# Performance work log

Measured on AMD Instinct MI355X. Metric: run time of the kernel, lower is better.

## Reference

```python
import jax, jax.numpy as jnp
import numpy as np

CLIP_LENGTH = 256.0
NUM_CLASSES = 21
OVERLAP_THRESH = 0.5
GAMMA = 2.0
ALPHA = 0.25
EPS = float(np.finfo(np.float32).eps)

B, K, N_GT = 32, 32768, 32


def setup_inputs() -> dict:
    key = jax.random.key(0)
    ks = jax.random.split(key, 9)
    loc_data = jax.random.uniform(ks[0], (B, K, 2), jnp.float32) * 64.0 + 1.0  # frame-unit offsets
    conf_data = jax.random.normal(ks[1], (B, K, NUM_CLASSES), jnp.float32)
    prop_loc_data = jax.random.normal(ks[2], (B, K, 2), jnp.float32)
    prop_conf_data = jax.random.normal(ks[3], (B, K, NUM_CLASSES), jnp.float32)
    center_data = jax.random.normal(ks[4], (B, K, 1), jnp.float32)
    priors = jax.random.uniform(ks[5], (K, 1), jnp.float32)  # normalized centers in [0,1]
    t0 = jax.random.uniform(ks[6], (B, N_GT), jnp.float32) * 0.8
    dur = jax.random.uniform(ks[7], (B, N_GT), jnp.float32) * 0.18 + 0.02
    t1 = jnp.minimum(t0 + dur, 1.0)
    labels = jax.random.randint(ks[8], (B, N_GT), 1, NUM_CLASSES).astype(jnp.float32)
    targets = jnp.stack([t0, t1, labels], axis=-1)  # [B, N, 3]
    return {"loc_data": loc_data, "conf_data": conf_data, "prop_loc_data": prop_loc_data,
            "prop_conf_data": prop_conf_data, "center_data": center_data,
            "priors": priors, "targets": targets}


def _calc_iou(pred, target):
    pl, pr = pred[..., 0], pred[..., 1]
    tl, tr = target[..., 0], target[..., 1]
    inter = jnp.minimum(pl, tl) + jnp.minimum(pr, tr)
    union = (pl + pr) + (tl + tr) - inter
    return inter / jnp.maximum(union, EPS)


def _giou_loss(pred, target):
    pl, pr = pred[..., 0], pred[..., 1]
    tl, tr = target[..., 0], target[..., 1]
    inter = jnp.minimum(pl, tl) + jnp.minimum(pr, tr)
    union = (pl + pr) + (tl + tr) - inter
    ious = inter / jnp.maximum(union, EPS)
    ac = jnp.maximum(pl, tl) + jnp.maximum(pr, tr)
    gious = ious - (ac - union) / jnp.maximum(ac, EPS)
    return 1.0 - gious


_ALPHA_VEC = jnp.full((NUM_CLASSES,), 1.0 - ALPHA, jnp.float32).at[0].set(ALPHA)


def _focal_sum(logits, tgt):
    # FocalLoss_Ori with pre-softmax inside MultiSegmentLoss; reduction=sum
    probs = jax.nn.softmax(logits, axis=-1)
    pt = jnp.take_along_axis(probs, tgt[..., None], axis=-1)[..., 0] + 1e-10
    return (-_ALPHA_VEC[tgt] * (1.0 - pt) ** GAMMA * jnp.log(pt)).sum()


def _match_targets(loc_data_ng, priors, targets):
    # everything here mirrors the torch.no_grad() matching block
    truths = targets[..., :2]                       # [B,N,2]
    labels = targets[..., 2].astype(jnp.int32)      # [B,N]
    center = priors[:, 0]                           # [K]
    left = (center[None, :, None] - truths[:, None, :, 0]) * CLIP_LENGTH   # [B,K,N]
    right = (truths[:, None, :, 1] - center[None, :, None]) * CLIP_LENGTH  # [B,K,N]
    maxn = CLIP_LENGTH * 2.0
    area = jnp.where((left < 0) | (right < 0), maxn, left + right)
    best_area = area.min(-1)                        # [B,K]
    best_idx = area.argmin(-1)                      # [B,K]
    t0 = jnp.take_along_axis(truths[..., 0], best_idx, axis=1)
    t1 = jnp.take_along_axis(truths[..., 1], best_idx, axis=1)
    loc_t = jnp.stack([(center[None, :] - t0) * CLIP_LENGTH,
                       (t1 - center[None, :]) * CLIP_LENGTH], axis=-1)     # [B,K,2]
    conf_t = jnp.take_along_axis(labels, best_idx, axis=1)
    conf_t = jnp.where(best_area >= maxn, 0, conf_t)                       # [B,K]
    iou = _calc_iou(loc_data_ng, loc_t)
    prop_conf_t = jnp.where(iou < OVERLAP_THRESH, 0, conf_t)
    prop_w = loc_data_ng[..., 0] + loc_data_ng[..., 1]
    prop_loc_t = (loc_t - loc_data_ng) / (0.5 * prop_w[..., None])
    return loc_t, conf_t, prop_loc_t, prop_conf_t


def reference(loc_data, conf_data, prop_loc_data, prop_conf_data, center_data, priors, targets):
    loc_t, conf_t, prop_loc_t, prop_conf_t = _match_targets(
        jax.lax.stop_gradient(loc_data), priors, targets)

    pos = conf_t > 0
    posf = pos.astype(loc_data.dtype)
    N = jnp.maximum(posf.sum(), 1.0)
    prop_pos = prop_conf_t > 0
    ppf = prop_pos.astype(loc_data.dtype)
    PN = jnp.maximum(ppf.sum(), 1.0)

    # GIoU localization loss over positives
    loss_l = (_giou_loss(loc_data, loc_t) * posf).sum() / N

    # L1 proposal refinement loss over proposal positives
    loss_prop_l = (jnp.abs(prop_loc_data - prop_loc_t).sum(-1) * ppf).sum() / PN

    # centerness BCE-with-logits against refined IoU, over positives
    prop_pre_w = loc_data[..., 0:1] + loc_data[..., 1:2]
    cur_loc_p = 0.5 * prop_pre_w * prop_loc_data + loc_data
    ious_ct = jnp.maximum(_calc_iou(cur_loc_p, loc_t), 0.0)
    x = center_data[..., 0]
    bce = jnp.maximum(x, 0.0) - x * ious_ct + jnp.log1p(jnp.exp(-jnp.abs(x)))
    loss_ct = (bce * posf).sum() / N

    # focal classification losses over all anchors
    loss_c = _focal_sum(conf_data, conf_t) / N
    loss_prop_c = _focal_sum(prop_conf_data, prop_conf_t) / PN

    return (loss_l, loss_c, loss_prop_l, loss_prop_c, loss_ct)
```

## Files before the change

### kernel.cpp

```cpp
#include <hip/hip_runtime.h>
#include <math.h>

#define NCLS 21
#define NGT 32
#define CLIPLEN 256.0f
#define MAXN 512.0f
#define FEPS 1.1920928955078125e-07f


typedef float f32x4 __attribute__((ext_vector_type(4)));
typedef f32x4 f32x4_u __attribute__((aligned(4)));

__device__ __forceinline__ float fastrcp(float x) { return __builtin_amdgcn_rcpf(x); }

__device__ __forceinline__ void load_row21(const float* __restrict__ p, float* r) {
    f32x4 v0 = *(const f32x4_u*)(p + 0);
    f32x4 v1 = *(const f32x4_u*)(p + 4);
    f32x4 v2 = *(const f32x4_u*)(p + 8);
    f32x4 v3 = *(const f32x4_u*)(p + 12);
    f32x4 v4 = *(const f32x4_u*)(p + 16);
    float  v5 = p[20];
    r[0]=v0.x; r[1]=v0.y; r[2]=v0.z; r[3]=v0.w;
    r[4]=v1.x; r[5]=v1.y; r[6]=v1.z; r[7]=v1.w;
    r[8]=v2.x; r[9]=v2.y; r[10]=v2.z; r[11]=v2.w;
    r[12]=v3.x; r[13]=v3.y; r[14]=v3.z; r[15]=v3.w;
    r[16]=v4.x; r[17]=v4.y; r[18]=v4.z; r[19]=v4.w;
    r[20]=v5;
}

__device__ __forceinline__ float focal_reg(const float* r, int tgt) {
    float m0 = fmaxf(fmaxf(r[0],  r[1]),  r[2]);
    float m1 = fmaxf(fmaxf(r[3],  r[4]),  r[5]);
    float m2 = fmaxf(fmaxf(r[6],  r[7]),  r[8]);
    float m3 = fmaxf(fmaxf(r[9],  r[10]), r[11]);
    float m4 = fmaxf(fmaxf(r[12], r[13]), r[14]);
    float m5 = fmaxf(fmaxf(r[15], r[16]), r[17]);
    float m6 = fmaxf(fmaxf(r[18], r[19]), r[20]);
    float ma = fmaxf(fmaxf(m0, m1), m2);
    float mb = fmaxf(fmaxf(m3, m4), m5);
    float m  = fmaxf(fmaxf(ma, mb), m6);

    float e[NCLS];
#pragma unroll
    for (int i = 0; i < NCLS; ++i) e[i] = __expf(r[i] - m);
    float s0 = (e[0] + e[1])  + (e[2] + e[3]);
    float s1 = (e[4] + e[5])  + (e[6] + e[7]);
    float s2 = (e[8] + e[9])  + (e[10] + e[11]);
    float s3 = (e[12] + e[13]) + (e[14] + e[15]);
    float s4 = (e[16] + e[17]) + (e[18] + e[19]);
    float s  = ((s0 + s1) + (s2 + s3)) + (s4 + e[20]);

    float rt = 0.0f;
#pragma unroll
    for (int i = 0; i < NCLS; ++i) rt = (i == tgt) ? r[i] : rt;

    float pt  = __expf(rt - m) * fastrcp(s) + 1e-10f;
    float lpt = __logf(pt);
    float a   = (tgt == 0) ? 0.25f : 0.75f;
    float om  = 1.0f - pt;
    return -a * om * om * lpt;
}

template <bool PARTIALS>
__global__ __launch_bounds__(256, 5) void msl_main(
    const float* __restrict__ loc_data,
    const float* __restrict__ conf_data,
    const float* __restrict__ prop_loc_data,
    const float* __restrict__ prop_conf_data,
    const float* __restrict__ center_data,
    const float* __restrict__ priors,
    const float* __restrict__ targets,
    double* __restrict__ ws,
    int K, int nblk)
{
    __shared__ float s_red[6 * 4];

    const int b    = blockIdx.y;
    const int tid  = threadIdx.x;
    const int lane = tid & 63;
    const int w    = tid >> 6;
    const int k    = blockIdx.x * 256 + tid;
    const size_t idx = (size_t)b * K + k;

    const float  c   = priors[k];
    const float2 loc = ((const float2*)loc_data)[idx];
    const float2 plo = ((const float2*)prop_loc_data)[idx];
    const float  x   = center_data[idx];

    float rc[NCLS], rp[NCLS];
    load_row21(conf_data      + idx * NCLS, rc);
    load_row21(prop_conf_data + idx * NCLS, rp);

    const float* tgs = targets + (size_t)b * (NGT * 3);
    float bestA = 3.0e38f;
    float bT0 = 0.0f, bT1 = 0.0f, bLb = 0.0f;
#pragma unroll
    for (int n = 0; n < NGT; ++n) {
        const float t0n = tgs[3 * n];
        const float t1n = tgs[3 * n + 1];
        const float lbn = tgs[3 * n + 2];
        const bool outside = (t0n > c) || (t1n < c);
        const float cand = outside ? MAXN : (t1n - t0n) * CLIPLEN;
        const bool better = cand < bestA;
        bestA = better ? cand : bestA;
        bT0   = better ? t0n  : bT0;
        bT1   = better ? t1n  : bT1;
        bLb   = better ? lbn  : bLb;
    }
    const float tl = (c - bT0) * CLIPLEN;
    const float tr = (bT1 - c) * CLIPLEN;
    const int conf_t = (bestA >= MAXN) ? 0 : (int)bLb;

    const float pl = loc.x, pr = loc.y;

    const float inter = fminf(pl, tl) + fminf(pr, tr);
    const float uni   = pl + pr + tl + tr - inter;
    const float iou   = inter * fastrcp(fmaxf(uni, FEPS));

    const int prop_conf_t = (iou < 0.5f) ? 0 : conf_t;
    const float posf = (conf_t > 0) ? 1.0f : 0.0f;
    const float ppf  = (prop_conf_t > 0) ? 1.0f : 0.0f;

    const float ac   = fmaxf(pl, tl) + fmaxf(pr, tr);
    const float giou = iou - (ac - uni) * fastrcp(fmaxf(ac, FEPS));
    const float v_ll = (1.0f - giou) * posf;

    const float prop_w = pl + pr;
    const float inv_hw = 2.0f * fastrcp(prop_w);
    const float plt0 = (tl - pl) * inv_hw;
    const float plt1 = (tr - pr) * inv_hw;
    const float v_lpl = (fabsf(plo.x - plt0) + fabsf(plo.y - plt1)) * ppf;

    const float cur0 = 0.5f * prop_w * plo.x + pl;
    const float cur1 = 0.5f * prop_w * plo.y + pr;
    const float in2  = fminf(cur0, tl) + fminf(cur1, tr);
    const float un2  = cur0 + cur1 + tl + tr - in2;
    const float iou2 = fmaxf(in2 * fastrcp(fmaxf(un2, FEPS)), 0.0f);
    const float ebx  = __expf(-fabsf(x));
    const float bce  = fmaxf(x, 0.0f) - x * iou2 + __logf(1.0f + ebx);
    const float v_ct = bce * posf;

    const float v_lc  = focal_reg(rc, conf_t);
    const float v_lpc = focal_reg(rp, prop_conf_t);

    float vals[6] = { v_ll, v_lc, v_lpl, v_lpc, v_ct, posf + 4096.0f * ppf };
#pragma unroll
    for (int i = 0; i < 6; ++i) {
        float v = vals[i];
#pragma unroll
        for (int off = 32; off > 0; off >>= 1) v += __shfl_xor(v, off);
        if (lane == 0) s_red[i * 4 + w] = v;
    }
    __syncthreads();
    if (tid == 0) {
        const int blk = blockIdx.y * gridDim.x + blockIdx.x;
#pragma unroll
        for (int i = 0; i < 5; ++i) {
            double s = (double)s_red[i * 4 + 0] + (double)s_red[i * 4 + 1]
                     + (double)s_red[i * 4 + 2] + (double)s_red[i * 4 + 3];
            if (PARTIALS) ws[(size_t)i * nblk + blk] = s;
            else          atomicAdd(&ws[i], s);
        }
        double ct = (double)s_red[5 * 4 + 0] + (double)s_red[5 * 4 + 1]
                  + (double)s_red[5 * 4 + 2] + (double)s_red[5 * 4 + 3];
        double pp = floor(ct / 4096.0);
        double ps = ct - 4096.0 * pp;
        if (PARTIALS) {
            ws[(size_t)5 * nblk + blk] = ps;
            ws[(size_t)6 * nblk + blk] = pp;
        } else {
            atomicAdd(&ws[5], ps);
            atomicAdd(&ws[6], pp);
        }
    }
}

__global__ __launch_bounds__(256) void msl_reduce(
    const double* __restrict__ p, int nblk, float* __restrict__ out)
{
    __shared__ double s_acc[7];
    __shared__ double s_w[4];
    const int tid  = threadIdx.x;
    const int lane = tid & 63;
    const int w    = tid >> 6;

    for (int i = 0; i < 7; ++i) {
        double v = 0.0;
        for (int j = tid; j < nblk; j += 256) v += p[(size_t)i * nblk + j];
#pragma unroll
        for (int off = 32; off > 0; off >>= 1) v += __shfl_xor(v, off);
        if (lane == 0) s_w[w] = v;
        __syncthreads();
        if (tid == 0) s_acc[i] = s_w[0] + s_w[1] + s_w[2] + s_w[3];
        __syncthreads();
    }
    if (tid == 0) {
        const double N  = fmax(s_acc[5], 1.0);
        const double PN = fmax(s_acc[6], 1.0);
        out[0] = (float)(s_acc[0] / N);
        out[1] = (float)(s_acc[1] / N);
        out[2] = (float)(s_acc[2] / PN);
        out[3] = (float)(s_acc[3] / PN);
        out[4] = (float)(s_acc[4] / N);
    }
}

__global__ void msl_finalize(const double* __restrict__ acc, float* __restrict__ out) {
    const double N  = fmax(acc[5], 1.0);
    const double PN = fmax(acc[6], 1.0);
    out[0] = (float)(acc[0] / N);
    out[1] = (float)(acc[1] / N);
    out[2] = (float)(acc[2] / PN);
    out[3] = (float)(acc[3] / PN);
    out[4] = (float)(acc[4] / N);
}

extern "C" void kernel_launch(void* const* d_in, const int* in_sizes, int n_in,
                              void* d_out, int out_size, void* d_ws, size_t ws_size,
                              hipStream_t stream) {
    const float* loc_data       = (const float*)d_in[0];
    const float* conf_data      = (const float*)d_in[1];
    const float* prop_loc_data  = (const float*)d_in[2];
    const float* prop_conf_data = (const float*)d_in[3];
    const float* center_data    = (const float*)d_in[4];
    const float* priors         = (const float*)d_in[5];
    const float* targets        = (const float*)d_in[6];
    float* out = (float*)d_out;

    const int K = in_sizes[5];
    const int B = in_sizes[6] / (NGT * 3);
    const int nblk = (K / 256) * B;

    double* ws = (double*)d_ws;
    dim3 grid(K / 256, B);

    if (ws_size >= (size_t)7 * nblk * sizeof(double)) {
        msl_main<true><<<grid, 256, 0, stream>>>(loc_data, conf_data, prop_loc_data,
                                                 prop_conf_data, center_data, priors,
                                                 targets, ws, K, nblk);
        msl_reduce<<<1, 256, 0, stream>>>(ws, nblk, out);
    } else {
        hipMemsetAsync(ws, 0, 7 * sizeof(double), stream);
        msl_main<false><<<grid, 256, 0, stream>>>(loc_data, conf_data, prop_loc_data,
                                                  prop_conf_data, center_data, priors,
                                                  targets, ws, K, nblk);
        msl_finalize<<<1, 1, 0, stream>>>(ws, out);
    }
}
```

Measured before the change: 69.03 us.

## Process four batch slices per thread with double-buffered register prefetch

The main kernel is replaced by one where each thread handles the same anchor across four batch slices. It loads the next slice's rows into a second register buffer while computing the current one, so memory latency is software-pipelined. This cuts the block count and the number of partial sums by four, and the prior value is reused across slices. In exchange, register pressure roughly doubles (launch bounds drop to 3 waves per SIMD), which may lower occupancy. A separate fallback kernel with the atomic path is kept for shapes that do not divide evenly.

```diff
diff --git a/kernel.cpp b/kernel.cpp
--- a/kernel.cpp
+++ b/kernel.cpp
@@ -3,6 +3,7 @@
 
 #define NCLS 21
 #define NGT 32
+#define NITER 4
 #define CLIPLEN 256.0f
 #define MAXN 512.0f
 #define FEPS 1.1920928955078125e-07f
@@ -61,37 +62,10 @@
     return -a * om * om * lpt;
 }
 
-template <bool PARTIALS>
-__global__ __launch_bounds__(256, 5) void msl_main(
-    const float* __restrict__ loc_data,
-    const float* __restrict__ conf_data,
-    const float* __restrict__ prop_loc_data,
-    const float* __restrict__ prop_conf_data,
-    const float* __restrict__ center_data,
-    const float* __restrict__ priors,
-    const float* __restrict__ targets,
-    double* __restrict__ ws,
-    int K, int nblk)
+__device__ __forceinline__ void anchor_accum(
+    const float* __restrict__ tgs, float c, float2 loc, float2 plo, float x,
+    const float* rc, const float* rp, float* a6)
 {
-    __shared__ float s_red[6 * 4];
-
-    const int b    = blockIdx.y;
-    const int tid  = threadIdx.x;
-    const int lane = tid & 63;
-    const int w    = tid >> 6;
-    const int k    = blockIdx.x * 256 + tid;
-    const size_t idx = (size_t)b * K + k;
-
-    const float  c   = priors[k];
-    const float2 loc = ((const float2*)loc_data)[idx];
-    const float2 plo = ((const float2*)prop_loc_data)[idx];
-    const float  x   = center_data[idx];
-
-    float rc[NCLS], rp[NCLS];
-    load_row21(conf_data      + idx * NCLS, rc);
-    load_row21(prop_conf_data + idx * NCLS, rp);
-
-    const float* tgs = targets + (size_t)b * (NGT * 3);
     float bestA = 3.0e38f;
     float bT0 = 0.0f, bT1 = 0.0f, bLb = 0.0f;
 #pragma unroll
@@ -140,38 +114,156 @@
     const float bce  = fmaxf(x, 0.0f) - x * iou2 + __logf(1.0f + ebx);
     const float v_ct = bce * posf;
 
-    const float v_lc  = focal_reg(rc, conf_t);
-    const float v_lpc = focal_reg(rp, prop_conf_t);
-
-    float vals[6] = { v_ll, v_lc, v_lpl, v_lpc, v_ct, posf + 4096.0f * ppf };
+    a6[0] += v_ll;
+    a6[1] += focal_reg(rc, conf_t);
+    a6[2] += v_lpl;
+    a6[3] += focal_reg(rp, prop_conf_t);
+    a6[4] += v_ct;
+    a6[5] += posf + 4096.0f * ppf;
+}
+
+__global__ __launch_bounds__(256, 3) void msl_pipe(
+    const float* __restrict__ loc_data,
+    const float* __restrict__ conf_data,
+    const float* __restrict__ prop_loc_data,
+    const float* __restrict__ prop_conf_data,
+    const float* __restrict__ center_data,
+    const float* __restrict__ priors,
+    const float* __restrict__ targets,
+    double* __restrict__ ws,
+    int K, int GB, int nblk)
+{
+    __shared__ float s_red[6 * 4];
+
+    const int tid  = threadIdx.x;
+    const int lane = tid & 63;
+    const int w    = tid >> 6;
+    const int T    = blockIdx.x * 256 + tid;
+    const int b0   = T / K;
+    const int k    = T - b0 * K;
+    const size_t step = (size_t)GB * K;
+
+    const float c = priors[k];
+
+    float rcA[NCLS], rpA[NCLS], rcB[NCLS], rpB[NCLS];
+    float2 locA, ploA, locB, ploB;
+    float xA, xB;
+    float a6[6] = {0, 0, 0, 0, 0, 0};
+
+    const size_t i0 = (size_t)T;
+    locA = ((const float2*)loc_data)[i0];
+    ploA = ((const float2*)prop_loc_data)[i0];
+    xA   = center_data[i0];
+    load_row21(conf_data      + i0 * NCLS, rcA);
+    load_row21(prop_conf_data + i0 * NCLS, rpA);
+
+    {
+        const size_t i1 = i0 + step;
+        locB = ((const float2*)loc_data)[i1];
+        ploB = ((const float2*)prop_loc_data)[i1];
+        xB   = center_data[i1];
+        load_row21(conf_data      + i1 * NCLS, rcB);
+        load_row21(prop_conf_data + i1 * NCLS, rpB);
+        anchor_accum(targets + (size_t)b0 * (NGT * 3), c, locA, ploA, xA, rcA, rpA, a6);
+    }
+    {
+        const size_t i2 = i0 + 2 * step;
+        locA = ((const float2*)loc_data)[i2];
+        ploA = ((const float2*)prop_loc_data)[i2];
+        xA   = center_data[i2];
+        load_row21(conf_data      + i2 * NCLS, rcA);
+        load_row21(prop_conf_data + i2 * NCLS, rpA);
+        anchor_accum(targets + (size_t)(b0 + GB) * (NGT * 3), c, locB, ploB, xB, rcB, rpB, a6);
+    }
+    {
+        const size_t i3 = i0 + 3 * step;
+        locB = ((const float2*)loc_data)[i3];
+        ploB = ((const float2*)prop_loc_data)[i3];
+        xB   = center_data[i3];
+        load_row21(conf_data      + i3 * NCLS, rcB);
+        load_row21(prop_conf_data + i3 * NCLS, rpB);
+        anchor_accum(targets + (size_t)(b0 + 2 * GB) * (NGT * 3), c, locA, ploA, xA, rcA, rpA, a6);
+    }
+    anchor_accum(targets + (size_t)(b0 + 3 * GB) * (NGT * 3), c, locB, ploB, xB, rcB, rpB, a6);
+
 #pragma unroll
     for (int i = 0; i < 6; ++i) {
-        float v = vals[i];
+        float v = a6[i];
 #pragma unroll
         for (int off = 32; off > 0; off >>= 1) v += __shfl_xor(v, off);
         if (lane == 0) s_red[i * 4 + w] = v;
     }
     __syncthreads();
     if (tid == 0) {
-        const int blk = blockIdx.y * gridDim.x + blockIdx.x;
+        const int blk = blockIdx.x;
 #pragma unroll
         for (int i = 0; i < 5; ++i) {
             double s = (double)s_red[i * 4 + 0] + (double)s_red[i * 4 + 1]
                      + (double)s_red[i * 4 + 2] + (double)s_red[i * 4 + 3];
-            if (PARTIALS) ws[(size_t)i * nblk + blk] = s;
-            else          atomicAdd(&ws[i], s);
+            ws[(size_t)i * nblk + blk] = s;
         }
         double ct = (double)s_red[5 * 4 + 0] + (double)s_red[5 * 4 + 1]
                   + (double)s_red[5 * 4 + 2] + (double)s_red[5 * 4 + 3];
         double pp = floor(ct / 4096.0);
         double ps = ct - 4096.0 * pp;
-        if (PARTIALS) {
-            ws[(size_t)5 * nblk + blk] = ps;
-            ws[(size_t)6 * nblk + blk] = pp;
-        } else {
-            atomicAdd(&ws[5], ps);
-            atomicAdd(&ws[6], pp);
+        ws[(size_t)5 * nblk + blk] = ps;
+        ws[(size_t)6 * nblk + blk] = pp;
+    }
+}
+
+__global__ __launch_bounds__(256, 8) void msl_fallback(
+    const float* __restrict__ loc_data,
+    const float* __restrict__ conf_data,
+    const float* __restrict__ prop_loc_data,
+    const float* __restrict__ prop_conf_data,
+    const float* __restrict__ center_data,
+    const float* __restrict__ priors,
+    const float* __restrict__ targets,
+    double* __restrict__ ws,
+    int K)
+{
+    __shared__ float s_red[6 * 4];
+    const int tid  = threadIdx.x;
+    const int lane = tid & 63;
+    const int w    = tid >> 6;
+    const int kxPerB = K >> 8;
+    const int b  = blockIdx.x / kxPerB;
+    const int kx = blockIdx.x - b * kxPerB;
+    const int k  = kx * 256 + tid;
+    const size_t idx = (size_t)b * K + k;
+
+    const float  c   = priors[k];
+    const float2 loc = ((const float2*)loc_data)[idx];
+    const float2 plo = ((const float2*)prop_loc_data)[idx];
+    const float  x   = center_data[idx];
+    float rc[NCLS], rp[NCLS];
+    load_row21(conf_data      + idx * NCLS, rc);
+    load_row21(prop_conf_data + idx * NCLS, rp);
+
+    float a6[6] = {0, 0, 0, 0, 0, 0};
+    anchor_accum(targets + (size_t)b * (NGT * 3), c, loc, plo, x, rc, rp, a6);
+
+#pragma unroll
+    for (int i = 0; i < 6; ++i) {
+        float v = a6[i];
+#pragma unroll
+        for (int off = 32; off > 0; off >>= 1) v += __shfl_xor(v, off);
+        if (lane == 0) s_red[i * 4 + w] = v;
+    }
+    __syncthreads();
+    if (tid == 0) {
+#pragma unroll
+        for (int i = 0; i < 5; ++i) {
+            double s = (double)s_red[i * 4 + 0] + (double)s_red[i * 4 + 1]
+                     + (double)s_red[i * 4 + 2] + (double)s_red[i * 4 + 3];
+            atomicAdd(&ws[i], s);
         }
+        double ct = (double)s_red[5 * 4 + 0] + (double)s_red[5 * 4 + 1]
+                  + (double)s_red[5 * 4 + 2] + (double)s_red[5 * 4 + 3];
+        double pp = floor(ct / 4096.0);
+        double ps = ct - 4096.0 * pp;
+        atomicAdd(&ws[5], ps);
+        atomicAdd(&ws[6], pp);
     }
 }
 
@@ -229,21 +321,23 @@
 
     const int K = in_sizes[5];
     const int B = in_sizes[6] / (NGT * 3);
-    const int nblk = (K / 256) * B;
 
     double* ws = (double*)d_ws;
-    dim3 grid(K / 256, B);
-
-    if (ws_size >= (size_t)7 * nblk * sizeof(double)) {
-        msl_main<true><<<grid, 256, 0, stream>>>(loc_data, conf_data, prop_loc_data,
-                                                 prop_conf_data, center_data, priors,
-                                                 targets, ws, K, nblk);
-        msl_reduce<<<1, 256, 0, stream>>>(ws, nblk, out);
-    } else {
-        hipMemsetAsync(ws, 0, 7 * sizeof(double), stream);
-        msl_main<false><<<grid, 256, 0, stream>>>(loc_data, conf_data, prop_loc_data,
-                                                  prop_conf_data, center_data, priors,
-                                                  targets, ws, K, nblk);
-        msl_finalize<<<1, 1, 0, stream>>>(ws, out);
-    }
-}
+
+    const bool pipeOK = (B % NITER == 0) && (((long)(B / NITER) * K) % 256 == 0);
+    if (pipeOK) {
+        const int GB   = B / NITER;
+        const int nblk = (int)(((long)GB * K) / 256);
+        if (ws_size >= (size_t)7 * nblk * sizeof(double)) {
+            msl_pipe<<<dim3(nblk), 256, 0, stream>>>(loc_data, conf_data, prop_loc_data,
+                                                     prop_conf_data, center_data, priors,
+                                                     targets, ws, K, GB, nblk);
+            msl_reduce<<<1, 256, 0, stream>>>(ws, nblk, out);
+            return;
+        }
+    }
+    hipMemsetAsync(ws, 0, 7 * sizeof(double), stream);
+    msl_fallback<<<dim3((K / 256) * B), 256, 0, stream>>>(loc_data, conf_data,
+        prop_loc_data, prop_conf_data, center_data, priors, targets, ws, K);
+    msl_finalize<<<1, 1, 0, stream>>>(ws, out);
+}
```

Result: slower. 122.3 us (+77.1%).
